# Kernel tuning notes

Hardware: AMD Instinct MI355X
Metric: run time of the kernel (lower is better)

The kernel has to match this reference:

```python
import jax, jax.numpy as jnp
import numpy as np

N = 100000      # nodes
E = 640000      # total edges across all relations
D_IN = 128
D_OUT = 128
R = 8           # num_rel
B = 4           # num_bases


def setup_inputs() -> dict:
    key = jax.random.key(0)
    ks = jax.random.split(key, 7)
    return {
        "X": jax.random.normal(ks[0], (N, D_IN), dtype=jnp.float32),
        "edge_src": jax.random.randint(ks[1], (E,), 0, N, dtype=jnp.int32),
        "edge_dst": jax.random.randint(ks[2], (E,), 0, N, dtype=jnp.int32),
        "edge_rel": jax.random.randint(ks[3], (E,), 0, R, dtype=jnp.int32),
        "edge_val": jax.random.uniform(ks[4], (E,), dtype=jnp.float32),
        "w_bases": jax.random.normal(ks[5], (B, D_IN, D_OUT), dtype=jnp.float32) * 0.05,
        "w_rel": jax.random.normal(ks[6], (R, B), dtype=jnp.float32) * 0.5,
    }


def reference(X, edge_src, edge_dst, edge_rel, edge_val, w_bases, w_rel):
    # Per-relation SpMM: support_r = A_r @ X, where A_r rows are destinations.
    # Fuse all relations into one gather + one segmented scatter-add.
    msg = X[edge_src] * edge_val[:, None]                      # [E, D_IN]
    seg = edge_rel.astype(jnp.int32) * N + edge_dst            # combined (rel, dst) id
    supports = jax.ops.segment_sum(msg, seg, num_segments=R * N)
    supports = supports.reshape(R, N, D_IN)                    # == concat of per-rel supports
    # Basis-decomposed relation weights: w[r] = sum_b w_rel[r,b] * w_bases[b]
    w = jnp.einsum("rb,bio->rio", w_rel, w_bases)              # [R, D_IN, D_OUT]
    # cat(supports, dim=1) @ w.view(R*D_IN, D_OUT) == sum_r supports_r @ w_r
    out = jnp.einsum("rni,rio->no", supports, w)               # [N, D_OUT]
    return out
```

## Files before the change

### kernel.cpp

```cpp
#include <hip/hip_runtime.h>
#include <stdint.h>

#define D_IN 128
#define D_OUT 128
#define NREL 8
#define NBASE 4

typedef __attribute__((ext_vector_type(8))) short short8;
typedef __attribute__((ext_vector_type(4))) float floatx4;
typedef __attribute__((ext_vector_type(2))) float floatx2;

__device__ __forceinline__ unsigned short f2bf(float f) {
  unsigned int u = __float_as_uint(f);
  u += 0x7fffu + ((u >> 16) & 1u);
  return (unsigned short)(u >> 16);
}
__device__ __forceinline__ unsigned pack2bf(float lo, float hi) {
  return (unsigned)f2bf(lo) | ((unsigned)f2bf(hi) << 16);
}
__device__ __forceinline__ float bflo(unsigned int u) { return __uint_as_float(u << 16); }
__device__ __forceinline__ float bfhi(unsigned int u) { return __uint_as_float(u & 0xffff0000u); }

__global__ void k_prep(const float4* __restrict__ X, ushort4* __restrict__ Xb, int n4,
                       const float* __restrict__ w_bases, unsigned short* __restrict__ W2T,
                       uint4* __restrict__ counts4, int nc4) {
  int i = blockIdx.x * blockDim.x + threadIdx.x;
  if (i < n4) {
    float4 v = X[i];
    ushort4 o;
    o.x = f2bf(v.x); o.y = f2bf(v.y); o.z = f2bf(v.z); o.w = f2bf(v.w);
    Xb[i] = o;
  }
  if (i < 128 * 512) {
    int o = i >> 9, c = i & 511;
    int k = c >> 2, b = c & 3;
    W2T[i] = f2bf(w_bases[(b * D_IN + k) * D_OUT + o]);
  }
  if (i < nc4) counts4[i] = make_uint4(0u, 0u, 0u, 0u);
}

__global__ void k_count(const int* __restrict__ dst, int* __restrict__ counts, int E) {
  int i = blockIdx.x * blockDim.x + threadIdx.x;
  if (i < E) atomicAdd(&counts[dst[i]], 1);
}

__global__ void k_scan1(const int* __restrict__ counts, int* __restrict__ localsc,
                        int* __restrict__ bsum, int Nn) {
  __shared__ int s[256];
  int i = blockIdx.x * 256 + threadIdx.x;
  int v = (i < Nn) ? counts[i] : 0;
  s[threadIdx.x] = v;
  __syncthreads();
  for (int off = 1; off < 256; off <<= 1) {
    int t = 0;
    if (threadIdx.x >= off) t = s[threadIdx.x - off];
    __syncthreads();
    s[threadIdx.x] += t;
    __syncthreads();
  }
  if (i < Nn) localsc[i] = s[threadIdx.x] - v;
  if (threadIdx.x == 255) bsum[blockIdx.x] = s[255];
}

__global__ void k_scan23(const int* __restrict__ localsc, const int* __restrict__ bsum,
                         int* __restrict__ offsets, int* __restrict__ cursor, int Nn, int E) {
  __shared__ int red[256];
  int acc = 0;
  for (int j = threadIdx.x; j < blockIdx.x; j += 256) acc += bsum[j];
  red[threadIdx.x] = acc;
  __syncthreads();
  for (int off = 128; off > 0; off >>= 1) {
    if (threadIdx.x < off) red[threadIdx.x] += red[threadIdx.x + off];
    __syncthreads();
  }
  int pref = red[0];
  int i = blockIdx.x * 256 + threadIdx.x;
  if (i < Nn) {
    int v = localsc[i] + pref;
    offsets[i] = v;
    cursor[i] = v;
  }
  if (i == 0) offsets[Nn] = E;
}

__global__ void k_bucket(const int* __restrict__ src, const int* __restrict__ dst,
                         const int* __restrict__ rel, const float* __restrict__ val,
                         int* __restrict__ cursor, uint2* __restrict__ bucket, int E) {
  int i = blockIdx.x * blockDim.x + threadIdx.x;
  if (i >= E) return;
  int d = dst[i];
  int pos = atomicAdd(&cursor[d], 1);
  bucket[pos] = make_uint2((unsigned)src[i] | ((unsigned)rel[i] << 21), __float_as_uint(val[i]));
}

__global__ __launch_bounds__(256)
void k_agg_gemm(const uint2* __restrict__ bucket, const int* __restrict__ offsets,
                const float* __restrict__ w_rel_g, const unsigned* __restrict__ Xb2,
                const unsigned short* __restrict__ W2T, float* __restrict__ out, int Nn) {
  __shared__ __align__(16) unsigned short aggS[32][520];
  __shared__ __align__(16) float wrS[NREL * NBASE];
  if (threadIdx.x < NREL * NBASE) wrS[threadIdx.x] = w_rel_g[threadIdx.x];
  __syncthreads();

  const int wave = threadIdx.x >> 6, lane = threadIdx.x & 63;
  const int d0 = blockIdx.x * 32 + wave * 8;
  const floatx2 zf2 = {0.f, 0.f};

  int oidx = d0 + (lane < 8 ? lane : 8);
  if (oidx > Nn) oidx = Nn;
  const int offv = offsets[oidx];
  const int s0 = __shfl(offv, 0);
  const int e8 = __shfl(offv, 8);

  floatx2 a0 = zf2, a1 = zf2, a2 = zf2, a3 = zf2;
  int row = 0;
  int bnd = __shfl(offv, 1);

#define FLUSH()                                                      \
  do {                                                               \
    uint4 o_;                                                        \
    o_.x = pack2bf(a0.x, a1.x);                                      \
    o_.y = pack2bf(a2.x, a3.x);                                      \
    o_.z = pack2bf(a0.y, a1.y);                                      \
    o_.w = pack2bf(a2.y, a3.y);                                      \
    *(uint4*)&aggS[wave * 8 + row][lane * 8] = o_;                   \
    a0 = zf2; a1 = zf2; a2 = zf2; a3 = zf2;                          \
    ++row;                                                           \
    bnd = (row < 8) ? __shfl(offv, row + 1) : 0x7fffffff;            \
  } while (0)

#define ACCT(EI, R, V, Y)                                            \
  do {                                                               \
    if ((EI) < e8) {                                                 \
      while ((EI) == bnd) FLUSH();                                   \
      const float4 w_ = *(const float4*)&wrS[((R) >> 21) * 4];       \
      const float val_ = __uint_as_float(V);                         \
      const float c0_ = val_ * w_.x, c1_ = val_ * w_.y;              \
      const float c2_ = val_ * w_.z, c3_ = val_ * w_.w;              \
      floatx2 x_;                                                    \
      x_.x = bflo(Y);                                                \
      x_.y = bfhi(Y);                                                \
      a0 += c0_ * x_;                                                \
      a1 += c1_ * x_;                                                \
      a2 += c2_ * x_;                                                \
      a3 += c3_ * x_;                                                \
    }                                                                \
  } while (0)

#define LOADG(P, BASE)                                               \
  do {                                                               \
    const int gb_ = (BASE);                                          \
    if (gb_ - cbase >= 64) {                                         \
      cbase += 64;                                                   \
      chC = chN;                                                     \
      int in_ = cbase + 64 + lane;                                   \
      if (in_ > ce) in_ = ce;                                        \
      chN = bucket[in_];                                             \
    }                                                                \
    const int j0_ = gb_ - cbase;                                     \
    int t1_ = gb_ + 1; if (t1_ > ce) t1_ = ce;                       \
    int t2_ = gb_ + 2; if (t2_ > ce) t2_ = ce;                       \
    int t3_ = gb_ + 3; if (t3_ > ce) t3_ = ce;                       \
    const int j1_ = t1_ - cbase, j2_ = t2_ - cbase, j3_ = t3_ - cbase; \
    r##P##0 = __shfl(chC.x, j0_); v##P##0 = __shfl(chC.y, j0_);      \
    r##P##1 = __shfl(chC.x, j1_); v##P##1 = __shfl(chC.y, j1_);      \
    r##P##2 = __shfl(chC.x, j2_); v##P##2 = __shfl(chC.y, j2_);      \
    r##P##3 = __shfl(chC.x, j3_); v##P##3 = __shfl(chC.y, j3_);      \
    y##P##0 = Xb2[((size_t)(r##P##0 & 0x1FFFFFu) << 6) + lane];      \
    y##P##1 = Xb2[((size_t)(r##P##1 & 0x1FFFFFu) << 6) + lane];      \
    y##P##2 = Xb2[((size_t)(r##P##2 & 0x1FFFFFu) << 6) + lane];      \
    y##P##3 = Xb2[((size_t)(r##P##3 & 0x1FFFFFu) << 6) + lane];      \
  } while (0)

  if (s0 < e8) {
    const int ce = e8 - 1;
    int cbase = s0;
    uint2 chC, chN;
    {
      int i0 = cbase + lane;
      if (i0 > ce) i0 = ce;
      chC = bucket[i0];
      int i1 = cbase + 64 + lane;
      if (i1 > ce) i1 = ce;
      chN = bucket[i1];
    }
    unsigned rA0, rA1, rA2, rA3, vA0, vA1, vA2, vA3, yA0, yA1, yA2, yA3;
    unsigned rB0, rB1, rB2, rB3, vB0, vB1, vB2, vB3, yB0, yB1, yB2, yB3;
    LOADG(A, s0);
    int gi = s0;
    int par = 0;
    while (gi < e8) {
      const int gn = gi + 4;
      if (par == 0) {
        if (gn < e8) LOADG(B, gn);
        ACCT(gi, rA0, vA0, yA0);
        ACCT(gi + 1, rA1, vA1, yA1);
        ACCT(gi + 2, rA2, vA2, yA2);
        ACCT(gi + 3, rA3, vA3, yA3);
      } else {
        if (gn < e8) LOADG(A, gn);
        ACCT(gi, rB0, vB0, yB0);
        ACCT(gi + 1, rB1, vB1, yB1);
        ACCT(gi + 2, rB2, vB2, yB2);
        ACCT(gi + 3, rB3, vB3, yB3);
      }
      par ^= 1;
      gi = gn;
    }
  }
  while (row < 8) FLUSH();

  __syncthreads();

  const int q = lane >> 4, r16 = lane & 15;
  const int wn = wave * 32;
  const floatx4 zero = {0.f, 0.f, 0.f, 0.f};
  floatx4 acc[2][2];
  acc[0][0] = zero; acc[0][1] = zero; acc[1][0] = zero; acc[1][1] = zero;

#pragma unroll 4
  for (int k0 = 0; k0 < 512; k0 += 32) {
    int ka = k0 + q * 8;
    short8 af[2], bfv[2];
    af[0] = *(const short8*)&aggS[r16][ka];
    af[1] = *(const short8*)&aggS[16 + r16][ka];
    bfv[0] = *(const short8*)(W2T + (size_t)(wn + r16) * 512 + ka);
    bfv[1] = *(const short8*)(W2T + (size_t)(wn + 16 + r16) * 512 + ka);
#pragma unroll
    for (int i = 0; i < 2; ++i)
#pragma unroll
      for (int j = 0; j < 2; ++j)
        acc[i][j] = __builtin_amdgcn_mfma_f32_16x16x32_bf16(af[i], bfv[j], acc[i][j], 0, 0, 0);
  }

#pragma unroll
  for (int i = 0; i < 2; ++i) {
#pragma unroll
    for (int j = 0; j < 2; ++j) {
#pragma unroll
      for (int p = 0; p < 4; ++p) {
        int prow = i * 16 + q * 4 + p;
        int col = wn + j * 16 + r16;
        int grow = blockIdx.x * 32 + prow;
        if (grow < Nn) out[(size_t)grow * 128 + col] = acc[i][j][p];
      }
    }
  }
}

extern "C" void kernel_launch(void* const* d_in, const int* in_sizes, int n_in,
                              void* d_out, int out_size, void* d_ws, size_t ws_size,
                              hipStream_t stream) {
  const float* X = (const float*)d_in[0];
  const int* esrc = (const int*)d_in[1];
  const int* edst = (const int*)d_in[2];
  const int* erel = (const int*)d_in[3];
  const float* eval_ = (const float*)d_in[4];
  const float* w_bases = (const float*)d_in[5];
  const float* w_rel = (const float*)d_in[6];
  const int Nn = in_sizes[0] / D_IN;
  const int E = in_sizes[1];

  char* ws = (char*)d_ws;
  size_t off = 0;
  auto alloc = [&](size_t bytes) -> char* {
    char* p = ws + off;
    off += (bytes + 255) & ~(size_t)255;
    return p;
  };
  unsigned short* Xb = (unsigned short*)alloc((size_t)Nn * D_IN * 2);
  unsigned short* W2T = (unsigned short*)alloc((size_t)128 * 512 * 2);
  int* counts = (int*)alloc((size_t)Nn * 4);
  int* cursor = (int*)alloc((size_t)Nn * 4);
  int* offsets = (int*)alloc((size_t)(Nn + 1) * 4);
  int* localsc = (int*)alloc((size_t)Nn * 4);
  int* bsum = (int*)alloc(4096);
  uint2* bucket = (uint2*)alloc((size_t)E * 8);
  (void)ws_size;

  int n4 = Nn * D_IN / 4;
  int nc4 = Nn / 4;
  k_prep<<<(n4 + 255) / 256, 256, 0, stream>>>((const float4*)X, (ushort4*)Xb, n4,
                                               w_bases, W2T, (uint4*)counts, nc4);

  k_count<<<(E + 255) / 256, 256, 0, stream>>>(edst, counts, E);
  int nb = (Nn + 255) / 256;
  k_scan1<<<nb, 256, 0, stream>>>(counts, localsc, bsum, Nn);
  k_scan23<<<nb, 256, 0, stream>>>(localsc, bsum, offsets, cursor, Nn, E);
  k_bucket<<<(E + 255) / 256, 256, 0, stream>>>(esrc, edst, erel, eval_, cursor, bucket, E);

  k_agg_gemm<<<(Nn + 31) / 32, 256, 0, stream>>>(bucket, offsets, w_rel,
                                                 (const unsigned*)Xb, W2T,
                                                 (float*)d_out, Nn);
}
```

Before: 264.0 us.

## Deepen gather prefetch to four stages and shrink agg-gemm blocks to 16 rows

The aggregation loop now keeps three groups of four gathered X rows in flight instead of one, which hides more gather latency in the edge loop. Blocks shrink from 256 to 128 threads covering 16 destination rows, so there are more, smaller blocks and less LDS per block. Each wave now computes a 16x64 output tile with four MFMAs per k-step. Offset broadcasts use readlane instead of shuffles. The cost is higher register pressure from the extra prefetch buffers and more redundant W2T reads across the larger number of blocks.

```diff
diff --git a/kernel.cpp b/kernel.cpp
--- a/kernel.cpp
+++ b/kernel.cpp
@@ -93,28 +93,29 @@
   bucket[pos] = make_uint2((unsigned)src[i] | ((unsigned)rel[i] << 21), __float_as_uint(val[i]));
 }
 
-__global__ __launch_bounds__(256)
+__global__ __launch_bounds__(128)
 void k_agg_gemm(const uint2* __restrict__ bucket, const int* __restrict__ offsets,
                 const float* __restrict__ w_rel_g, const unsigned* __restrict__ Xb2,
                 const unsigned short* __restrict__ W2T, float* __restrict__ out, int Nn) {
-  __shared__ __align__(16) unsigned short aggS[32][520];
+  __shared__ __align__(16) unsigned short aggS[16][520];
   __shared__ __align__(16) float wrS[NREL * NBASE];
   if (threadIdx.x < NREL * NBASE) wrS[threadIdx.x] = w_rel_g[threadIdx.x];
   __syncthreads();
 
   const int wave = threadIdx.x >> 6, lane = threadIdx.x & 63;
-  const int d0 = blockIdx.x * 32 + wave * 8;
+  const int d0 = blockIdx.x * 16 + wave * 8;
+  const unsigned* __restrict__ Xl = Xb2 + lane;
   const floatx2 zf2 = {0.f, 0.f};
 
   int oidx = d0 + (lane < 8 ? lane : 8);
   if (oidx > Nn) oidx = Nn;
   const int offv = offsets[oidx];
-  const int s0 = __shfl(offv, 0);
-  const int e8 = __shfl(offv, 8);
+  const int s0 = __builtin_amdgcn_readlane(offv, 0);
+  const int e8 = __builtin_amdgcn_readlane(offv, 8);
 
   floatx2 a0 = zf2, a1 = zf2, a2 = zf2, a3 = zf2;
   int row = 0;
-  int bnd = __shfl(offv, 1);
+  int bnd = __builtin_amdgcn_readlane(offv, 1);
 
 #define FLUSH()                                                      \
   do {                                                               \
@@ -126,7 +127,8 @@
     *(uint4*)&aggS[wave * 8 + row][lane * 8] = o_;                   \
     a0 = zf2; a1 = zf2; a2 = zf2; a3 = zf2;                          \
     ++row;                                                           \
-    bnd = (row < 8) ? __shfl(offv, row + 1) : 0x7fffffff;            \
+    bnd = (row < 8) ? __builtin_amdgcn_readlane(offv, row + 1)       \
+                    : 0x7fffffff;                                    \
   } while (0)
 
 #define ACCT(EI, R, V, Y)                                            \
@@ -149,27 +151,27 @@
 
 #define LOADG(P, BASE)                                               \
   do {                                                               \
-    const int gb_ = (BASE);                                          \
-    if (gb_ - cbase >= 64) {                                         \
+    int t0_ = (BASE); if (t0_ > ce) t0_ = ce;                        \
+    if (t0_ - cbase >= 64) {                                         \
       cbase += 64;                                                   \
       chC = chN;                                                     \
       int in_ = cbase + 64 + lane;                                   \
       if (in_ > ce) in_ = ce;                                        \
       chN = bucket[in_];                                             \
     }                                                                \
-    const int j0_ = gb_ - cbase;                                     \
-    int t1_ = gb_ + 1; if (t1_ > ce) t1_ = ce;                       \
-    int t2_ = gb_ + 2; if (t2_ > ce) t2_ = ce;                       \
-    int t3_ = gb_ + 3; if (t3_ > ce) t3_ = ce;                       \
-    const int j1_ = t1_ - cbase, j2_ = t2_ - cbase, j3_ = t3_ - cbase; \
+    int t1_ = (BASE) + 1; if (t1_ > ce) t1_ = ce;                    \
+    int t2_ = (BASE) + 2; if (t2_ > ce) t2_ = ce;                    \
+    int t3_ = (BASE) + 3; if (t3_ > ce) t3_ = ce;                    \
+    const int j0_ = t0_ - cbase, j1_ = t1_ - cbase;                  \
+    const int j2_ = t2_ - cbase, j3_ = t3_ - cbase;                  \
     r##P##0 = __shfl(chC.x, j0_); v##P##0 = __shfl(chC.y, j0_);      \
     r##P##1 = __shfl(chC.x, j1_); v##P##1 = __shfl(chC.y, j1_);      \
     r##P##2 = __shfl(chC.x, j2_); v##P##2 = __shfl(chC.y, j2_);      \
     r##P##3 = __shfl(chC.x, j3_); v##P##3 = __shfl(chC.y, j3_);      \
-    y##P##0 = Xb2[((size_t)(r##P##0 & 0x1FFFFFu) << 6) + lane];      \
-    y##P##1 = Xb2[((size_t)(r##P##1 & 0x1FFFFFu) << 6) + lane];      \
-    y##P##2 = Xb2[((size_t)(r##P##2 & 0x1FFFFFu) << 6) + lane];      \
-    y##P##3 = Xb2[((size_t)(r##P##3 & 0x1FFFFFu) << 6) + lane];      \
+    y##P##0 = Xl[(r##P##0 & 0x1FFFFFu) << 6];                        \
+    y##P##1 = Xl[(r##P##1 & 0x1FFFFFu) << 6];                        \
+    y##P##2 = Xl[(r##P##2 & 0x1FFFFFu) << 6];                        \
+    y##P##3 = Xl[(r##P##3 & 0x1FFFFFu) << 6];                        \
   } while (0)
 
   if (s0 < e8) {
@@ -186,26 +188,34 @@
     }
     unsigned rA0, rA1, rA2, rA3, vA0, vA1, vA2, vA3, yA0, yA1, yA2, yA3;
     unsigned rB0, rB1, rB2, rB3, vB0, vB1, vB2, vB3, yB0, yB1, yB2, yB3;
+    unsigned rC0, rC1, rC2, rC3, vC0, vC1, vC2, vC3, yC0, yC1, yC2, yC3;
+    unsigned rD0, rD1, rD2, rD3, vD0, vD1, vD2, vD3, yD0, yD1, yD2, yD3;
     LOADG(A, s0);
+    LOADG(B, s0 + 4);
+    LOADG(C, s0 + 8);
     int gi = s0;
-    int par = 0;
     while (gi < e8) {
-      const int gn = gi + 4;
-      if (par == 0) {
-        if (gn < e8) LOADG(B, gn);
-        ACCT(gi, rA0, vA0, yA0);
-        ACCT(gi + 1, rA1, vA1, yA1);
-        ACCT(gi + 2, rA2, vA2, yA2);
-        ACCT(gi + 3, rA3, vA3, yA3);
-      } else {
-        if (gn < e8) LOADG(A, gn);
-        ACCT(gi, rB0, vB0, yB0);
-        ACCT(gi + 1, rB1, vB1, yB1);
-        ACCT(gi + 2, rB2, vB2, yB2);
-        ACCT(gi + 3, rB3, vB3, yB3);
-      }
-      par ^= 1;
-      gi = gn;
+      LOADG(D, gi + 12);
+      ACCT(gi, rA0, vA0, yA0);
+      ACCT(gi + 1, rA1, vA1, yA1);
+      ACCT(gi + 2, rA2, vA2, yA2);
+      ACCT(gi + 3, rA3, vA3, yA3);
+      LOADG(A, gi + 16);
+      ACCT(gi + 4, rB0, vB0, yB0);
+      ACCT(gi + 5, rB1, vB1, yB1);
+      ACCT(gi + 6, rB2, vB2, yB2);
+      ACCT(gi + 7, rB3, vB3, yB3);
+      LOADG(B, gi + 20);
+      ACCT(gi + 8, rC0, vC0, yC0);
+      ACCT(gi + 9, rC1, vC1, yC1);
+      ACCT(gi + 10, rC2, vC2, yC2);
+      ACCT(gi + 11, rC3, vC3, yC3);
+      LOADG(C, gi + 24);
+      ACCT(gi + 12, rD0, vD0, yD0);
+      ACCT(gi + 13, rD1, vD1, yD1);
+      ACCT(gi + 14, rD2, vD2, yD2);
+      ACCT(gi + 15, rD3, vD3, yD3);
+      gi += 16;
     }
   }
   while (row < 8) FLUSH();
@@ -213,37 +223,32 @@
   __syncthreads();
 
   const int q = lane >> 4, r16 = lane & 15;
-  const int wn = wave * 32;
+  const int wn = wave * 64;
   const floatx4 zero = {0.f, 0.f, 0.f, 0.f};
-  floatx4 acc[2][2];
-  acc[0][0] = zero; acc[0][1] = zero; acc[1][0] = zero; acc[1][1] = zero;
+  floatx4 acc[4];
+  acc[0] = zero; acc[1] = zero; acc[2] = zero; acc[3] = zero;
 
 #pragma unroll 4
   for (int k0 = 0; k0 < 512; k0 += 32) {
     int ka = k0 + q * 8;
-    short8 af[2], bfv[2];
-    af[0] = *(const short8*)&aggS[r16][ka];
-    af[1] = *(const short8*)&aggS[16 + r16][ka];
-    bfv[0] = *(const short8*)(W2T + (size_t)(wn + r16) * 512 + ka);
-    bfv[1] = *(const short8*)(W2T + (size_t)(wn + 16 + r16) * 512 + ka);
+    short8 af = *(const short8*)&aggS[r16][ka];
+    short8 bfv[4];
 #pragma unroll
-    for (int i = 0; i < 2; ++i)
+    for (int j = 0; j < 4; ++j)
+      bfv[j] = *(const short8*)(W2T + (size_t)(wn + j * 16 + r16) * 512 + ka);
 #pragma unroll
-      for (int j = 0; j < 2; ++j)
-        acc[i][j] = __builtin_amdgcn_mfma_f32_16x16x32_bf16(af[i], bfv[j], acc[i][j], 0, 0, 0);
+    for (int j = 0; j < 4; ++j)
+      acc[j] = __builtin_amdgcn_mfma_f32_16x16x32_bf16(af, bfv[j], acc[j], 0, 0, 0);
   }
 
 #pragma unroll
-  for (int i = 0; i < 2; ++i) {
+  for (int j = 0; j < 4; ++j) {
 #pragma unroll
-    for (int j = 0; j < 2; ++j) {
-#pragma unroll
-      for (int p = 0; p < 4; ++p) {
-        int prow = i * 16 + q * 4 + p;
-        int col = wn + j * 16 + r16;
-        int grow = blockIdx.x * 32 + prow;
-        if (grow < Nn) out[(size_t)grow * 128 + col] = acc[i][j][p];
-      }
+    for (int p = 0; p < 4; ++p) {
+      int prow = q * 4 + p;
+      int col = wn + j * 16 + r16;
+      int grow = blockIdx.x * 16 + prow;
+      if (grow < Nn) out[(size_t)grow * 128 + col] = acc[j][p];
     }
   }
 }
@@ -289,7 +294,7 @@
   k_scan23<<<nb, 256, 0, stream>>>(localsc, bsum, offsets, cursor, Nn, E);
   k_bucket<<<(E + 255) / 256, 256, 0, stream>>>(esrc, edst, erel, eval_, cursor, bucket, E);
 
-  k_agg_gemm<<<(Nn + 31) / 32, 256, 0, stream>>>(bucket, offsets, w_rel,
+  k_agg_gemm<<<(Nn + 15) / 16, 128, 0, stream>>>(bucket, offsets, w_rel,
                                                  (const unsigned*)Xb, W2T,
                                                  (float*)d_out, Nn);
 }
```

Result: slower. 290.3 us (+10.0%).
